# Performance work log

Hardware: AMD Instinct MI355X
Metric: run time of the kernel (lower is better)

## Reference

```python
import jax, jax.numpy as jnp
import numpy as np

N, E, G = 50000, 800000, 64
F_IN, HID = 128, 128


def setup_inputs() -> dict:
    key = jax.random.key(0)
    ks = jax.random.split(key, 8)
    x = jax.random.normal(ks[0], (N, F_IN), dtype=jnp.float32)
    edge_index = jax.random.randint(ks[1], (2, E), 0, N, dtype=jnp.int32)
    batch = jnp.sort(jax.random.randint(ks[2], (N,), 0, G, dtype=jnp.int32))
    def glorot(k, shape):
        fan = shape[0] + shape[1]
        return jax.random.normal(k, shape, dtype=jnp.float32) * jnp.sqrt(2.0 / fan)
    return {
        "x": x,
        "edge_index": edge_index,
        "batch": batch,
        "W0": glorot(ks[3], (F_IN, HID)), "b0": jnp.zeros((HID,), jnp.float32),
        "W1": glorot(ks[4], (HID, HID)), "b1": jnp.zeros((HID,), jnp.float32),
        "W2": glorot(ks[5], (HID, HID)), "b2": jnp.zeros((HID,), jnp.float32),
        "fcW": glorot(ks[6], (HID, 1)), "fcb": jnp.zeros((1,), jnp.float32),
    }


def _gcn_graph_norm(edge_index, n):
    # add self loops, compute symmetric normalization D^-1/2 (A+I) D^-1/2
    loop = jnp.arange(n, dtype=edge_index.dtype)
    src = jnp.concatenate([edge_index[0], loop])
    dst = jnp.concatenate([edge_index[1], loop])
    deg = jax.ops.segment_sum(jnp.ones_like(dst, dtype=jnp.float32), dst, num_segments=n)
    dis = jnp.where(deg > 0, jax.lax.rsqrt(jnp.maximum(deg, 1.0)), 0.0)
    norm = dis[src] * dis[dst]  # [E+N]
    return src, dst, norm


def _gcn_conv(x, W, b, src, dst, norm, n):
    h = x @ W                                 # [N, H] dense transform first (cheaper)
    msg = h[src] * norm[:, None]              # gather + scale  [E+N, H]
    out = jax.ops.segment_sum(msg, dst, num_segments=n)  # scatter-add
    return out + b


def reference(x, edge_index, batch, W0, b0, W1, b1, W2, b2, fcW, fcb):
    n = x.shape[0]
    src, dst, norm = _gcn_graph_norm(edge_index, n)
    h = _gcn_conv(x, W0, b0, src, dst, norm, n)
    h = jax.nn.relu(h)  # dropout is identity in eval mode
    h = _gcn_conv(h, W1, b1, src, dst, norm, n)
    h = jax.nn.relu(h)
    h = _gcn_conv(h, W2, b2, src, dst, norm, n)
    # global mean pool over graphs
    sums = jax.ops.segment_sum(h, batch, num_segments=G)          # [G, H]
    cnts = jax.ops.segment_sum(jnp.ones((n,), jnp.float32), batch, num_segments=G)
    pooled = sums / jnp.maximum(cnts, 1.0)[:, None]
    return (pooled @ fcW + fcb).squeeze(-1)  # [G]
```

## Files before the change

### kernel.cpp

```cpp
#include <hip/hip_runtime.h>
#include <hip/hip_bf16.h>
#include <hip/hip_fp16.h>

#define NTHREADS 256
#define GTHREADS 512
#define POOL_CHUNK 32
#define BKT_EDGES 4096
#define CAP 8192

typedef __attribute__((ext_vector_type(8))) short short8;
typedef __attribute__((ext_vector_type(4))) float f32x4;

__device__ __forceinline__ unsigned short f32_bf16(float f) {
  unsigned u = __float_as_uint(f);
  u += 0x7FFF + ((u >> 16) & 1);
  return (unsigned short)(u >> 16);
}
__device__ __forceinline__ float bf16_f32(unsigned short h) {
  return __uint_as_float((unsigned)h << 16);
}


__global__ __launch_bounds__(NTHREADS) void prep_w_kernel(
    const float* __restrict__ W0, const float* __restrict__ W1,
    const float* __restrict__ W2, unsigned short* __restrict__ wt_hi,
    unsigned short* __restrict__ wt_lo, int* __restrict__ cursor,
    float* __restrict__ sums, int NB, int sums_len) {
  int idx = blockIdx.x * NTHREADS + threadIdx.x;
  if (idx < NB) cursor[idx] = idx * CAP;
  if (idx < sums_len) sums[idx] = 0.f;
  int w = idx >> 14;
  int e = idx & 16383;
  int c = e >> 7, k = e & 127;
  const float* W = (w == 0) ? W0 : ((w == 1) ? W1 : W2);
  float v = W[k * 128 + c];
  unsigned short hi = f32_bf16(v);
  unsigned short lo = f32_bf16(v - bf16_f32(hi));
  size_t off = (size_t)w * 16384 + (k >> 3) * 1024 + c * 8 + (k & 7);
  wt_hi[off] = hi;
  wt_lo[off] = lo;
}


__global__ __launch_bounds__(NTHREADS) void bucketize_kernel(
    const int* __restrict__ src, const int* __restrict__ dst,
    int* __restrict__ cursor, unsigned* __restrict__ store, int E) {
  __shared__ unsigned packed[BKT_EDGES];
  __shared__ unsigned char bkt[BKT_EDGES];
  __shared__ int hist[256];
  __shared__ int base[256];
  const int tid = threadIdx.x;
  const int e0 = blockIdx.x * BKT_EDGES;
  const int cnt = min(BKT_EDGES, E - e0);

  hist[tid] = 0;
  __syncthreads();
  for (int i = tid; i < cnt; i += NTHREADS) {
    int s = src[e0 + i];
    int d = dst[e0 + i];
    packed[i] = ((unsigned)s << 8) | (unsigned)(d & 255);
    int b = d >> 8;
    bkt[i] = (unsigned char)b;
    atomicAdd(&hist[b], 1);
  }
  __syncthreads();
  int h = hist[tid];
  if (h) base[tid] = atomicAdd(&cursor[tid], h);
  __syncthreads();
  hist[tid] = 0;
  __syncthreads();
  for (int i = tid; i < cnt; i += NTHREADS) {
    int b = bkt[i];
    int off = atomicAdd(&hist[b], 1);
    int pos = base[b] + off;
    if (pos < (b + 1) * CAP) store[pos] = packed[i];
  }
}


__global__ __launch_bounds__(NTHREADS) void build_kernel(
    const unsigned* __restrict__ store, const int* __restrict__ cursor,
    int* __restrict__ rowptr, int* __restrict__ csr_src,
    float* __restrict__ dis, int n, int E, int NB) {
  __shared__ unsigned eb[CAP];
  __shared__ unsigned ord[CAP];
  __shared__ int bcnt[256];
  __shared__ int bscn[256];
  __shared__ int hist[256];
  __shared__ int scn[256];
  __shared__ int eoff[256];
  const int b = blockIdx.x;
  const int t = threadIdx.x;

  int bc = (t < NB) ? (cursor[t] - t * CAP) : 0;
  bcnt[t] = bc;
  bscn[t] = bc;
  __syncthreads();
  for (int off = 1; off < 256; off <<= 1) {
    int u = (t >= off) ? bscn[t - off] : 0;
    __syncthreads();
    bscn[t] += u;
    __syncthreads();
  }
  const int base = bscn[b] - bcnt[b];
  const int cnt = min(bcnt[b], CAP);

  for (int i = t; i < cnt; i += NTHREADS) eb[i] = store[(size_t)b * CAP + i];
  hist[t] = 0;
  __syncthreads();
  for (int i = t; i < cnt; i += NTHREADS) atomicAdd(&hist[eb[i] & 255u], 1);
  __syncthreads();

  const int node = b * 256 + t;
  const int deg = hist[t];
  if (node < n) dis[node] = rsqrtf((float)deg + 1.0f);

  scn[t] = deg;
  __syncthreads();
  for (int off = 1; off < 256; off <<= 1) {
    int u = (t >= off) ? scn[t - off] : 0;
    __syncthreads();
    scn[t] += u;
    __syncthreads();
  }
  int excl = scn[t] - deg;
  eoff[t] = excl;
  if (node <= n) rowptr[node] = base + excl;
  if (b == NB - 1 && t == 255) rowptr[n] = E;
  __syncthreads();
  hist[t] = 0;
  __syncthreads();
  for (int i = t; i < cnt; i += NTHREADS) {
    unsigned p = eb[i];
    int dl = p & 255u;
    int off = atomicAdd(&hist[dl], 1);
    ord[eoff[dl] + off] = p >> 8;
  }
  __syncthreads();
  for (int i = t; i < cnt; i += NTHREADS) csr_src[base + i] = (int)ord[i];
}


template <bool BF16_IN>
__global__ __launch_bounds__(GTHREADS) void gemm_mfma_kernel(
    const void* __restrict__ in_, const unsigned short* __restrict__ wt_hi,
    const unsigned short* __restrict__ wt_lo, const float* __restrict__ dis,
    __half* __restrict__ hs, int n) {
  __shared__ unsigned short Whi[16384];
  __shared__ unsigned short Wlo[16384];
  const int tid = threadIdx.x;
  const int wave = tid >> 6, lane = tid & 63;
  const int g = lane >> 4, lr = lane & 15;

#pragma unroll
  for (int i = 0; i < 4; ++i) {
    int c = i * GTHREADS + tid;
    ((short8*)Whi)[c] = ((const short8*)wt_hi)[c];
    ((short8*)Wlo)[c] = ((const short8*)wt_lo)[c];
  }

  const int rowbase = blockIdx.x * 128 + wave * 16;
  const int arow = rowbase + lr;
  const int arow_c = (arow < n) ? arow : (n - 1);

  short8 a[4];
  if (BF16_IN) {
    const unsigned short* in = (const unsigned short*)in_;
#pragma unroll
    for (int ks = 0; ks < 4; ++ks) {
      union { short8 v; unsigned short u[8]; } t;
      t.v = *(const short8*)&in[(size_t)arow_c * 128 + ks * 32 + g * 8];
#pragma unroll
      for (int i = 0; i < 8; ++i) t.u[i] = (t.u[i] & 0x8000) ? 0 : t.u[i];
      a[ks] = t.v;
    }
  } else {
    const float* in = (const float*)in_;
#pragma unroll
    for (int ks = 0; ks < 4; ++ks) {
      union { short8 v; unsigned short u[8]; } t;
      const float* p = &in[(size_t)arow_c * 128 + ks * 32 + g * 8];
#pragma unroll
      for (int i = 0; i < 8; ++i) t.u[i] = f32_bf16(p[i]);
      a[ks] = t.v;
    }
  }

  __syncthreads();

  f32x4 acc[8];
#pragma unroll
  for (int ct = 0; ct < 8; ++ct) acc[ct] = (f32x4){0.f, 0.f, 0.f, 0.f};

#pragma unroll
  for (int ks = 0; ks < 4; ++ks) {
    const int kb = (ks * 4 + g) * 1024 + lr * 8;
    short8 bf[8];
#pragma unroll
    for (int ct = 0; ct < 8; ++ct) bf[ct] = *(const short8*)&Whi[kb + ct * 128];
#pragma unroll
    for (int ct = 0; ct < 8; ++ct)
      acc[ct] = __builtin_amdgcn_mfma_f32_16x16x32_bf16(a[ks], bf[ct], acc[ct], 0, 0, 0);
#pragma unroll
    for (int ct = 0; ct < 8; ++ct) bf[ct] = *(const short8*)&Wlo[kb + ct * 128];
#pragma unroll
    for (int ct = 0; ct < 8; ++ct)
      acc[ct] = __builtin_amdgcn_mfma_f32_16x16x32_bf16(a[ks], bf[ct], acc[ct], 0, 0, 0);
  }

  float dsv[4];
  int orow[4];
#pragma unroll
  for (int r = 0; r < 4; ++r) {
    orow[r] = rowbase + g * 4 + r;
    dsv[r] = (orow[r] < n) ? dis[orow[r]] : 0.f;
  }
#pragma unroll
  for (int ct = 0; ct < 8; ++ct) {
    int col = ct * 16 + lr;
#pragma unroll
    for (int r = 0; r < 4; ++r) {
      if (orow[r] < n)
        hs[(size_t)orow[r] * 128 + col] = __float2half(acc[ct][r] * dsv[r]);
    }
  }
}


__global__ __launch_bounds__(NTHREADS) void agg_kernel(
    const __half2* __restrict__ hs, const int* __restrict__ rowptr,
    const int* __restrict__ csr_src, const float* __restrict__ dis,
    const float* __restrict__ b, unsigned* __restrict__ out, int n) {
  int node = blockIdx.x * (NTHREADS / 64) + (threadIdx.x >> 6);
  int lane = threadIdx.x & 63;
  if (node >= n) return;
  int r0 = rowptr[node];
  int r1 = rowptr[node + 1];
  float di = dis[node];
  const char* hsb = (const char*)hs + lane * 4;

  float2 acc = __half22float2(hs[(size_t)node * 64 + lane]);
  float2 acc2 = make_float2(0.f, 0.f);
  float2 acc3 = make_float2(0.f, 0.f);
  float2 acc4 = make_float2(0.f, 0.f);

  int e = r0;
  for (; e + 15 < r1; e += 16) {
    int s[16];
#pragma unroll
    for (int j = 0; j < 16; ++j) s[j] = csr_src[e + j];
    __half2 v[16];
#pragma unroll
    for (int j = 0; j < 16; ++j)
      v[j] = *(const __half2*)(hsb + ((unsigned)s[j] << 8));
#pragma unroll
    for (int j = 0; j < 16; j += 4) {
      float2 f0 = __half22float2(v[j]);
      float2 f1 = __half22float2(v[j + 1]);
      float2 f2 = __half22float2(v[j + 2]);
      float2 f3 = __half22float2(v[j + 3]);
      acc.x += f0.x; acc.y += f0.y;
      acc2.x += f1.x; acc2.y += f1.y;
      acc3.x += f2.x; acc3.y += f2.y;
      acc4.x += f3.x; acc4.y += f3.y;
    }
  }
  for (; e + 3 < r1; e += 4) {
    int s0 = csr_src[e], s1 = csr_src[e + 1], s2 = csr_src[e + 2], s3 = csr_src[e + 3];
    float2 f0 = __half22float2(*(const __half2*)(hsb + ((unsigned)s0 << 8)));
    float2 f1 = __half22float2(*(const __half2*)(hsb + ((unsigned)s1 << 8)));
    float2 f2 = __half22float2(*(const __half2*)(hsb + ((unsigned)s2 << 8)));
    float2 f3 = __half22float2(*(const __half2*)(hsb + ((unsigned)s3 << 8)));
    acc.x += f0.x; acc.y += f0.y;
    acc2.x += f1.x; acc2.y += f1.y;
    acc3.x += f2.x; acc3.y += f2.y;
    acc4.x += f3.x; acc4.y += f3.y;
  }
  for (; e < r1; ++e) {
    int s0 = csr_src[e];
    float2 f0 = __half22float2(*(const __half2*)(hsb + ((unsigned)s0 << 8)));
    acc.x += f0.x; acc.y += f0.y;
  }
  acc.x += acc2.x + acc3.x + acc4.x;
  acc.y += acc2.y + acc3.y + acc4.y;

  float2 bb = *(const float2*)&b[lane * 2];
  float rx = fmaf(acc.x, di, bb.x);
  float ry = fmaf(acc.y, di, bb.y);
  unsigned lo = f32_bf16(rx);
  unsigned hi = f32_bf16(ry);
  out[(size_t)node * 64 + lane] = lo | (hi << 16);
}


__global__ __launch_bounds__(NTHREADS) void pool_kernel(
    const unsigned* __restrict__ h, const int* __restrict__ batch,
    float* __restrict__ sums, int n) {
  int wid = blockIdx.x * (NTHREADS / 64) + (threadIdx.x >> 6);
  int lane = threadIdx.x & 63;
  int i0 = wid * POOL_CHUNK;
  if (i0 >= n) return;
  int i1 = min(i0 + POOL_CHUNK, n);

  int g = batch[i0];
  float2 acc = make_float2(0.f, 0.f);
  for (int i = i0; i < i1; ++i) {
    int gi = batch[i];
    if (gi != g) {
      float* sp = &sums[g * 128 + lane * 2];
      atomicAdd(sp, acc.x);
      atomicAdd(sp + 1, acc.y);
      acc = make_float2(0.f, 0.f);
      g = gi;
    }
    unsigned v = h[(size_t)i * 64 + lane];
    acc.x += __uint_as_float(v << 16);
    acc.y += __uint_as_float(v & 0xFFFF0000u);
  }
  float* sp = &sums[g * 128 + lane * 2];
  atomicAdd(sp, acc.x);
  atomicAdd(sp + 1, acc.y);
}


__global__ __launch_bounds__(64) void fc_kernel(
    const float* __restrict__ sums, const int* __restrict__ batch,
    const float* __restrict__ fcW, const float* __restrict__ fcb,
    float* __restrict__ out, int n) {
  int g = blockIdx.x;
  int lane = threadIdx.x;
  float2 v = *(const float2*)&sums[g * 128 + lane * 2];
  float2 w = *(const float2*)&fcW[lane * 2];
  float p = v.x * w.x + v.y * w.y;
#pragma unroll
  for (int off = 32; off > 0; off >>= 1) p += __shfl_down(p, off);

  int lb = 0;
  if (lane < 2) {
    int key = g + lane;
    int lo = 0, hi = n;
    while (lo < hi) {
      int mid = (lo + hi) >> 1;
      if (batch[mid] < key) lo = mid + 1; else hi = mid;
    }
    lb = lo;
  }
  int lb0 = __shfl(lb, 0);
  int lb1 = __shfl(lb, 1);
  if (lane == 0) {
    float c = (float)(lb1 - lb0);
    out[g] = p / fmaxf(c, 1.0f) + fcb[0];
  }
}

extern "C" void kernel_launch(void* const* d_in, const int* in_sizes, int n_in,
                              void* d_out, int out_size, void* d_ws, size_t ws_size,
                              hipStream_t stream) {
  const float* x   = (const float*)d_in[0];
  const int* eidx  = (const int*)d_in[1];
  const int* batch = (const int*)d_in[2];
  const float* W0  = (const float*)d_in[3];
  const float* b0  = (const float*)d_in[4];
  const float* W1  = (const float*)d_in[5];
  const float* b1  = (const float*)d_in[6];
  const float* W2  = (const float*)d_in[7];
  const float* b2  = (const float*)d_in[8];
  const float* fcW = (const float*)d_in[9];
  const float* fcb = (const float*)d_in[10];
  float* out = (float*)d_out;

  const int N = in_sizes[0] / 128;
  const int E = in_sizes[1] / 2;
  const int G = out_size;
  const int NB = (N + 255) >> 8;

  const int* src = eidx;
  const int* dst = eidx + E;

  char* ws = (char*)d_ws;
  size_t off = 0;
  auto alloc = [&](size_t bytes) {
    void* p = ws + off;
    off = (off + bytes + 255) & ~(size_t)255;
    return p;
  };
  float*          dis    = (float*)         alloc((size_t)N * 4);
  int*            rowptr = (int*)           alloc((size_t)(N + 1) * 4);
  int*            cursor = (int*)           alloc((size_t)NB * 4);
  int*            csrsrc = (int*)           alloc((size_t)E * 4);
  unsigned*       store  = (unsigned*)      alloc((size_t)NB * CAP * 4);
  __half*         hsbuf  = (__half*)        alloc((size_t)N * 128 * 2);
  unsigned*       bufA   = (unsigned*)      alloc((size_t)N * 64 * 4);
  unsigned short* wt_hi  = (unsigned short*)alloc((size_t)3 * 16384 * 2);
  unsigned short* wt_lo  = (unsigned short*)alloc((size_t)3 * 16384 * 2);
  float*          sums   = (float*)         alloc((size_t)G * 128 * 4);

  prep_w_kernel<<<192, NTHREADS, 0, stream>>>(W0, W1, W2, wt_hi, wt_lo,
                                              cursor, sums, NB, G * 128);
  bucketize_kernel<<<(E + BKT_EDGES - 1) / BKT_EDGES, NTHREADS, 0, stream>>>(
      src, dst, cursor, store, E);
  build_kernel<<<NB, NTHREADS, 0, stream>>>(
      store, cursor, rowptr, csrsrc, dis, N, E, NB);

  const int gemm_blocks = (N + 127) / 128;
  const int node_blocks = (N + 3) / 4;
  const int pool_waves = (N + POOL_CHUNK - 1) / POOL_CHUNK;

  gemm_mfma_kernel<false><<<gemm_blocks, GTHREADS, 0, stream>>>(
      x, wt_hi, wt_lo, dis, hsbuf, N);
  agg_kernel<<<node_blocks, NTHREADS, 0, stream>>>(
      (const __half2*)hsbuf, rowptr, csrsrc, dis, b0, bufA, N);
  gemm_mfma_kernel<true><<<gemm_blocks, GTHREADS, 0, stream>>>(
      bufA, wt_hi + 16384, wt_lo + 16384, dis, hsbuf, N);
  agg_kernel<<<node_blocks, NTHREADS, 0, stream>>>(
      (const __half2*)hsbuf, rowptr, csrsrc, dis, b1, bufA, N);
  gemm_mfma_kernel<true><<<gemm_blocks, GTHREADS, 0, stream>>>(
      bufA, wt_hi + 32768, wt_lo + 32768, dis, hsbuf, N);
  agg_kernel<<<node_blocks, NTHREADS, 0, stream>>>(
      (const __half2*)hsbuf, rowptr, csrsrc, dis, b2, bufA, N);

  pool_kernel<<<(pool_waves + 3) / 4, NTHREADS, 0, stream>>>(bufA, batch, sums, N);
  fc_kernel<<<G, 64, 0, stream>>>(sums, batch, fcW, fcb, out, N);
}
```

Baseline: 197.8 us.

## Split wave into four edge groups with 16-byte row loads in aggregation

The aggregation kernel now splits each 64-lane wave into four groups of 16 lanes. Each group processes a different edge at the same time and loads a full 256-byte fp16 row using 16-byte vector loads, instead of one 4-byte load per lane per edge. Partial sums are combined with cross-lane shuffles, and 16 lanes write the output with 16-byte stores. This should cut the number of memory instructions and raise gather parallelism, at the cost of shuffle reductions and idle lanes in the tail and the final store.

```diff
diff --git a/kernel.cpp b/kernel.cpp
--- a/kernel.cpp
+++ b/kernel.cpp
@@ -18,6 +18,11 @@
 }
 __device__ __forceinline__ float bf16_f32(unsigned short h) {
   return __uint_as_float((unsigned)h << 16);
+}
+__device__ __forceinline__ float2 h2u(unsigned u) {
+  __half2 h;
+  *reinterpret_cast<unsigned*>(&h) = u;
+  return __half22float2(h);
 }
 
 
@@ -228,68 +233,96 @@
 
 
 __global__ __launch_bounds__(NTHREADS) void agg_kernel(
-    const __half2* __restrict__ hs, const int* __restrict__ rowptr,
+    const __half* __restrict__ hs, const int* __restrict__ rowptr,
     const int* __restrict__ csr_src, const float* __restrict__ dis,
     const float* __restrict__ b, unsigned* __restrict__ out, int n) {
   int node = blockIdx.x * (NTHREADS / 64) + (threadIdx.x >> 6);
   int lane = threadIdx.x & 63;
   if (node >= n) return;
-  int r0 = rowptr[node];
-  int r1 = rowptr[node + 1];
-  float di = dis[node];
-  const char* hsb = (const char*)hs + lane * 4;
-
-  float2 acc = __half22float2(hs[(size_t)node * 64 + lane]);
-  float2 acc2 = make_float2(0.f, 0.f);
-  float2 acc3 = make_float2(0.f, 0.f);
-  float2 acc4 = make_float2(0.f, 0.f);
+  const int rg = lane >> 4;
+  const int cl = lane & 15;
+  const int r0 = rowptr[node], r1 = rowptr[node + 1];
+  const float di = dis[node];
+
+  float2 a0 = {0.f, 0.f}, a1 = {0.f, 0.f}, a2 = {0.f, 0.f}, a3 = {0.f, 0.f};
+  float2 c0 = {0.f, 0.f}, c1 = {0.f, 0.f}, c2 = {0.f, 0.f}, c3 = {0.f, 0.f};
+
+  if (rg == 0) {
+    uint4 v = *(const uint4*)(hs + (size_t)node * 128 + cl * 8);
+    float2 f;
+    f = h2u(v.x); a0.x += f.x; a0.y += f.y;
+    f = h2u(v.y); a1.x += f.x; a1.y += f.y;
+    f = h2u(v.z); a2.x += f.x; a2.y += f.y;
+    f = h2u(v.w); a3.x += f.x; a3.y += f.y;
+  }
 
   int e = r0;
-  for (; e + 15 < r1; e += 16) {
-    int s[16];
-#pragma unroll
-    for (int j = 0; j < 16; ++j) s[j] = csr_src[e + j];
-    __half2 v[16];
-#pragma unroll
-    for (int j = 0; j < 16; ++j)
-      v[j] = *(const __half2*)(hsb + ((unsigned)s[j] << 8));
-#pragma unroll
-    for (int j = 0; j < 16; j += 4) {
-      float2 f0 = __half22float2(v[j]);
-      float2 f1 = __half22float2(v[j + 1]);
-      float2 f2 = __half22float2(v[j + 2]);
-      float2 f3 = __half22float2(v[j + 3]);
-      acc.x += f0.x; acc.y += f0.y;
-      acc2.x += f1.x; acc2.y += f1.y;
-      acc3.x += f2.x; acc3.y += f2.y;
-      acc4.x += f3.x; acc4.y += f3.y;
-    }
+  for (; e + 7 < r1; e += 8) {
+    int s0 = csr_src[e + rg];
+    int s1 = csr_src[e + 4 + rg];
+    uint4 v0 = *(const uint4*)(hs + (size_t)s0 * 128 + cl * 8);
+    uint4 v1 = *(const uint4*)(hs + (size_t)s1 * 128 + cl * 8);
+    float2 f;
+    f = h2u(v0.x); a0.x += f.x; a0.y += f.y;
+    f = h2u(v0.y); a1.x += f.x; a1.y += f.y;
+    f = h2u(v0.z); a2.x += f.x; a2.y += f.y;
+    f = h2u(v0.w); a3.x += f.x; a3.y += f.y;
+    f = h2u(v1.x); c0.x += f.x; c0.y += f.y;
+    f = h2u(v1.y); c1.x += f.x; c1.y += f.y;
+    f = h2u(v1.z); c2.x += f.x; c2.y += f.y;
+    f = h2u(v1.w); c3.x += f.x; c3.y += f.y;
   }
   for (; e + 3 < r1; e += 4) {
-    int s0 = csr_src[e], s1 = csr_src[e + 1], s2 = csr_src[e + 2], s3 = csr_src[e + 3];
-    float2 f0 = __half22float2(*(const __half2*)(hsb + ((unsigned)s0 << 8)));
-    float2 f1 = __half22float2(*(const __half2*)(hsb + ((unsigned)s1 << 8)));
-    float2 f2 = __half22float2(*(const __half2*)(hsb + ((unsigned)s2 << 8)));
-    float2 f3 = __half22float2(*(const __half2*)(hsb + ((unsigned)s3 << 8)));
-    acc.x += f0.x; acc.y += f0.y;
-    acc2.x += f1.x; acc2.y += f1.y;
-    acc3.x += f2.x; acc3.y += f2.y;
-    acc4.x += f3.x; acc4.y += f3.y;
-  }
-  for (; e < r1; ++e) {
-    int s0 = csr_src[e];
-    float2 f0 = __half22float2(*(const __half2*)(hsb + ((unsigned)s0 << 8)));
-    acc.x += f0.x; acc.y += f0.y;
-  }
-  acc.x += acc2.x + acc3.x + acc4.x;
-  acc.y += acc2.y + acc3.y + acc4.y;
-
-  float2 bb = *(const float2*)&b[lane * 2];
-  float rx = fmaf(acc.x, di, bb.x);
-  float ry = fmaf(acc.y, di, bb.y);
-  unsigned lo = f32_bf16(rx);
-  unsigned hi = f32_bf16(ry);
-  out[(size_t)node * 64 + lane] = lo | (hi << 16);
+    int s0 = csr_src[e + rg];
+    uint4 v0 = *(const uint4*)(hs + (size_t)s0 * 128 + cl * 8);
+    float2 f;
+    f = h2u(v0.x); a0.x += f.x; a0.y += f.y;
+    f = h2u(v0.y); a1.x += f.x; a1.y += f.y;
+    f = h2u(v0.z); a2.x += f.x; a2.y += f.y;
+    f = h2u(v0.w); a3.x += f.x; a3.y += f.y;
+  }
+  if (e < r1) {
+    int idx = e + rg;
+    if (idx < r1) {
+      int s0 = csr_src[idx];
+      uint4 v0 = *(const uint4*)(hs + (size_t)s0 * 128 + cl * 8);
+      float2 f;
+      f = h2u(v0.x); a0.x += f.x; a0.y += f.y;
+      f = h2u(v0.y); a1.x += f.x; a1.y += f.y;
+      f = h2u(v0.z); a2.x += f.x; a2.y += f.y;
+      f = h2u(v0.w); a3.x += f.x; a3.y += f.y;
+    }
+  }
+
+  a0.x += c0.x; a0.y += c0.y;
+  a1.x += c1.x; a1.y += c1.y;
+  a2.x += c2.x; a2.y += c2.y;
+  a3.x += c3.x; a3.y += c3.y;
+
+  a0.x += __shfl_down(a0.x, 32); a0.y += __shfl_down(a0.y, 32);
+  a1.x += __shfl_down(a1.x, 32); a1.y += __shfl_down(a1.y, 32);
+  a2.x += __shfl_down(a2.x, 32); a2.y += __shfl_down(a2.y, 32);
+  a3.x += __shfl_down(a3.x, 32); a3.y += __shfl_down(a3.y, 32);
+  a0.x += __shfl_down(a0.x, 16); a0.y += __shfl_down(a0.y, 16);
+  a1.x += __shfl_down(a1.x, 16); a1.y += __shfl_down(a1.y, 16);
+  a2.x += __shfl_down(a2.x, 16); a2.y += __shfl_down(a2.y, 16);
+  a3.x += __shfl_down(a3.x, 16); a3.y += __shfl_down(a3.y, 16);
+
+  if (lane < 16) {
+    const float* bp = &b[cl * 8];
+    float4 bb0 = *(const float4*)bp;
+    float4 bb1 = *(const float4*)(bp + 4);
+    uint4 w;
+    w.x = (unsigned)f32_bf16(fmaf(a0.x, di, bb0.x)) |
+          ((unsigned)f32_bf16(fmaf(a0.y, di, bb0.y)) << 16);
+    w.y = (unsigned)f32_bf16(fmaf(a1.x, di, bb0.z)) |
+          ((unsigned)f32_bf16(fmaf(a1.y, di, bb0.w)) << 16);
+    w.z = (unsigned)f32_bf16(fmaf(a2.x, di, bb1.x)) |
+          ((unsigned)f32_bf16(fmaf(a2.y, di, bb1.y)) << 16);
+    w.w = (unsigned)f32_bf16(fmaf(a3.x, di, bb1.z)) |
+          ((unsigned)f32_bf16(fmaf(a3.y, di, bb1.w)) << 16);
+    *(uint4*)(out + (size_t)node * 64 + cl * 4) = w;
+  }
 }
 
 
@@ -409,15 +442,15 @@
   gemm_mfma_kernel<false><<<gemm_blocks, GTHREADS, 0, stream>>>(
       x, wt_hi, wt_lo, dis, hsbuf, N);
   agg_kernel<<<node_blocks, NTHREADS, 0, stream>>>(
-      (const __half2*)hsbuf, rowptr, csrsrc, dis, b0, bufA, N);
+      hsbuf, rowptr, csrsrc, dis, b0, bufA, N);
   gemm_mfma_kernel<true><<<gemm_blocks, GTHREADS, 0, stream>>>(
       bufA, wt_hi + 16384, wt_lo + 16384, dis, hsbuf, N);
   agg_kernel<<<node_blocks, NTHREADS, 0, stream>>>(
-      (const __half2*)hsbuf, rowptr, csrsrc, dis, b1, bufA, N);
+      hsbuf, rowptr, csrsrc, dis, b1, bufA, N);
   gemm_mfma_kernel<true><<<gemm_blocks, GTHREADS, 0, stream>>>(
       bufA, wt_hi + 32768, wt_lo + 32768, dis, hsbuf, N);
   agg_kernel<<<node_blocks, NTHREADS, 0, stream>>>(
-      (const __half2*)hsbuf, rowptr, csrsrc, dis, b2, bufA, N);
+      hsbuf, rowptr, csrsrc, dis, b2, bufA, N);
 
   pool_kernel<<<(pool_waves + 3) / 4, NTHREADS, 0, stream>>>(bufA, batch, sums, N);
   fc_kernel<<<G, 64, 0, stream>>>(sums, batch, fcW, fcb, out, N);
```

After: 195.8 us. Within noise of the previous version (-1.0%).
